# Performance work log

Hardware: AMD Instinct MI355X
Metric: run time of the kernel (lower is better)

Reference implementation:

```python
import jax, jax.numpy as jnp
import numpy as np

B, T, S = 64, 50, 400
H, E, V = 512, 256, 50000
NB_UNK = 50

def setup_inputs() -> dict:
    key = jax.random.key(0)
    ks = jax.random.split(key, 20)
    sc = 0.05
    return {
        "input_token": jax.random.randint(ks[0], (B, 1), 0, V),
        "prev_decoder_h_states": jax.random.normal(ks[1], (B, T, H)) * 0.1,
        "last_hidden": jax.random.normal(ks[2], (B, H)) * 0.1,
        "encoder_states": jax.random.normal(ks[3], (B, S, H)) * 0.1,
        "full_input_var": jax.random.randint(ks[4], (B, S), 0, V + NB_UNK + 200),
        "previous_att": jax.random.normal(ks[5], (B, T, S)) * 0.1,
        "nb_unk_tokens": NB_UNK,
        "emb": jax.random.normal(ks[6], (V, E)) * sc,
        "W_ih": jax.random.normal(ks[7], (3 * H, E)) * sc,
        "W_hh": jax.random.normal(ks[8], (3 * H, H)) * sc,
        "b_ih": jax.random.normal(ks[9], (3 * H,)) * sc,
        "b_hh": jax.random.normal(ks[10], (3 * H,)) * sc,
        "w_h": jax.random.normal(ks[11], (H,)) * sc,
        "w_d": jax.random.normal(ks[12], (H,)) * sc,
        "W_oh": jax.random.normal(ks[13], (E, 3 * H)) * sc,
        "b_oh": jax.random.normal(ks[14], (E,)) * sc,
        "W_ov": jax.random.normal(ks[15], (V, E)) * sc,
        "b_ov": jax.random.normal(ks[16], (V,)) * sc,
        "W_gen": jax.random.normal(ks[17], (1, 3 * H)) * sc,
        "b_gen": jax.random.normal(ks[18], (1,)) * sc,
    }

def gru_step(x, h, W_ih, W_hh, b_ih, b_hh):
    # PyTorch GRU gate order: r, z, n
    gi = x @ W_ih.T + b_ih   # [B,3H]
    gh = h @ W_hh.T + b_hh   # [B,3H]
    i_r, i_z, i_n = jnp.split(gi, 3, axis=-1)
    h_r, h_z, h_n = jnp.split(gh, 3, axis=-1)
    r = jax.nn.sigmoid(i_r + h_r)
    z = jax.nn.sigmoid(i_z + h_z)
    n = jnp.tanh(i_n + r * h_n)
    return (1.0 - z) * n + z * h

def reference(input_token, prev_decoder_h_states, last_hidden, encoder_states,
              full_input_var, previous_att, nb_unk_tokens,
              emb, W_ih, W_hh, b_ih, b_hh, w_h, w_d,
              W_oh, b_oh, W_ov, b_ov, W_gen, b_gen):
    # embedding (dropout is identity at eval)
    x = emb[input_token[:, 0]]                                 # [B,E]
    h = gru_step(x, last_hidden, W_ih, W_hh, b_ih, b_hh)       # [B,H]

    # temporal (intra-temporal) encoder attention
    att_dist = jnp.einsum('bh,bsh->bs', h, w_h * encoder_states)      # [B,S]
    temporal = jnp.exp(att_dist) / jnp.exp(previous_att).sum(1)       # [B,S]
    new_previous_att = jnp.concatenate([previous_att, att_dist[:, None]], 1)
    att = temporal / temporal.sum(-1, keepdims=True)                   # [B,S]
    enc_ctx = jnp.einsum('bs,bsh->bh', att, encoder_states)           # [B,H]

    # intra-decoder attention
    dec_scores = jnp.einsum('bh,bth->bt', h, w_d * prev_decoder_h_states)
    dec_att = jax.nn.softmax(dec_scores, axis=-1)                      # [B,T]
    dec_ctx = jnp.einsum('bt,bth->bh', dec_att, prev_decoder_h_states)

    combined = jnp.concatenate([h, enc_ctx, dec_ctx], axis=-1)        # [B,3H]
    logits = (combined @ W_oh.T + b_oh) @ W_ov.T + b_ov               # [B,V]
    p_vocab = jax.nn.softmax(logits, axis=-1)
    p_gen = jax.nn.sigmoid(combined @ W_gen.T + b_gen)                # [B,1]

    # pointer copy distribution over extended vocab
    ext = V + nb_unk_tokens + 200
    bidx = jnp.arange(full_input_var.shape[0])[:, None]
    token_input_dist = jnp.zeros((full_input_var.shape[0], ext), dtype=att.dtype)
    token_input_dist = token_input_dist.at[bidx, full_input_var].add(att)

    pad = jnp.zeros((full_input_var.shape[0], nb_unk_tokens + 200), dtype=p_vocab.dtype)
    p_final = jnp.concatenate([p_vocab * p_gen, pad], axis=1) + (1.0 - p_gen) * token_input_dist

    decoder_h_states = jnp.concatenate([prev_decoder_h_states, h[:, None]], axis=1)
    return (p_final, p_gen, p_vocab, att, decoder_h_states, h, new_previous_att)
```

## Files before the change

kernel.cpp:

```cpp
#include <hip/hip_runtime.h>
#include <hip/hip_bf16.h>

#define B 64
#define T 50
#define S 400
#define H 512
#define E 256
#define V 50000
#define EXT 50250
#define G3 1536
#define NCH 32
#define NCE 8

typedef __attribute__((ext_vector_type(8))) short short8;
typedef __attribute__((ext_vector_type(4))) float f32x4;

#define O_PFINAL 0L
#define O_PGEN   3216000L
#define O_PVOCAB 3216064L
#define O_ATT    6416064L
#define O_DECH   6441664L
#define O_H      8112832L
#define O_NPA    8145600L

#define OFF_G      0L
#define OFF_GG     98304L
#define OFF_H      196608L
#define OFF_HW     229376L
#define OFF_HWD    262144L
#define OFF_ENCP   294912L
#define OFF_DEC    557056L
#define OFF_E      589824L
#define OFF_ESUM   615424L
#define OFF_PG     615936L
#define OFF_PROJBF 616064L
#define OFF_PSUM   624256L
#define OFF_TOK    1048576L

__device__ __forceinline__ float sigmoidf_(float x){ return 1.0f/(1.0f+expf(-x)); }
__device__ __forceinline__ short f2bs(float x){
    union { __hip_bfloat16 b; short s; } c; c.b = __float2bfloat16(x); return c.s;
}
__device__ __forceinline__ short8 cvt8(const float* p){
    f32x4 w0 = *(const f32x4*)p;
    f32x4 w1 = *(const f32x4*)(p + 4);
    short8 r;
    r[0]=f2bs(w0[0]); r[1]=f2bs(w0[1]); r[2]=f2bs(w0[2]); r[3]=f2bs(w0[3]);
    r[4]=f2bs(w1[0]); r[5]=f2bs(w1[1]); r[6]=f2bs(w1[2]); r[7]=f2bs(w1[3]);
    return r;
}

__global__ void k_prep(const float* pdh, const float* pa, float* out, float* tokd){
    const long n1 = (long)B*T*H/4, n2 = (long)B*T*S/4;
    const long nz = (long)B*EXT/4;
    long i0 = (long)blockIdx.x*256 + threadIdx.x;
    long stride = (long)gridDim.x*256;
    for (long i = i0; i < n1 + n2; i += stride){
        if (i < n1){
            long idx = i*4;
            int b = (int)(idx/(T*H)); int r = (int)(idx%(T*H)); int t = r/H; int k = r%H;
            *(f32x4*)(out + O_DECH + ((long)b*(T+1) + t)*H + k) = *(const f32x4*)(pdh + idx);
        } else {
            long idx = (i - n1)*4;
            int b = (int)(idx/(T*S)); int r = (int)(idx%(T*S)); int t = r/S; int s = r%S;
            *(f32x4*)(out + O_NPA + ((long)b*(T+1) + t)*S + s) = *(const f32x4*)(pa + idx);
        }
    }
    f32x4 z = {0.f,0.f,0.f,0.f};
    for (long i = i0; i < nz; i += stride)
        *(f32x4*)(tokd + i*4) = z;
}

__global__ void __launch_bounds__(128) k_gates(const int* tok,
                        const float* emb, const float* lh,
                        const float* Wih, const float* Whh,
                        const float* bih, const float* bhh,
                        float* g, float* Gg){
    int lane = threadIdx.x & 63, wave = threadIdx.x >> 6;
    int row = lane & 15, kg = lane >> 4;
    int j = blockIdx.x*16 + row;
    f32x4 c0={0.f,0.f,0.f,0.f}, c1={0.f,0.f,0.f,0.f};
    f32x4 c2={0.f,0.f,0.f,0.f}, c3={0.f,0.f,0.f,0.f};
    if (wave == 0){
        const float* Wp = Wih + (long)j*E + kg*8;
        const float* a0p = emb + (long)tok[row     ]*E + kg*8;
        const float* a1p = emb + (long)tok[row + 16]*E + kg*8;
        const float* a2p = emb + (long)tok[row + 32]*E + kg*8;
        const float* a3p = emb + (long)tok[row + 48]*E + kg*8;
        #pragma unroll
        for (int ks = 0; ks < 8; ks++){
            short8 bb = cvt8(Wp + ks*32);
            c0 = __builtin_amdgcn_mfma_f32_16x16x32_bf16(cvt8(a0p + ks*32), bb, c0, 0, 0, 0);
            c1 = __builtin_amdgcn_mfma_f32_16x16x32_bf16(cvt8(a1p + ks*32), bb, c1, 0, 0, 0);
            c2 = __builtin_amdgcn_mfma_f32_16x16x32_bf16(cvt8(a2p + ks*32), bb, c2, 0, 0, 0);
            c3 = __builtin_amdgcn_mfma_f32_16x16x32_bf16(cvt8(a3p + ks*32), bb, c3, 0, 0, 0);
        }
        float bi = bih[j];
        #pragma unroll
        for (int r = 0; r < 4; r++){
            int bg = kg*4 + r;
            g[(long)(bg     )*G3 + j] = c0[r] + bi;
            g[(long)(bg + 16)*G3 + j] = c1[r] + bi;
            g[(long)(bg + 32)*G3 + j] = c2[r] + bi;
            g[(long)(bg + 48)*G3 + j] = c3[r] + bi;
        }
    } else {
        const float* Wp = Whh + (long)j*H + kg*8;
        const float* a0p = lh + (long)(row     )*H + kg*8;
        const float* a1p = lh + (long)(row + 16)*H + kg*8;
        const float* a2p = lh + (long)(row + 32)*H + kg*8;
        const float* a3p = lh + (long)(row + 48)*H + kg*8;
        #pragma unroll
        for (int ks = 0; ks < 16; ks++){
            short8 bb = cvt8(Wp + ks*32);
            c0 = __builtin_amdgcn_mfma_f32_16x16x32_bf16(cvt8(a0p + ks*32), bb, c0, 0, 0, 0);
            c1 = __builtin_amdgcn_mfma_f32_16x16x32_bf16(cvt8(a1p + ks*32), bb, c1, 0, 0, 0);
            c2 = __builtin_amdgcn_mfma_f32_16x16x32_bf16(cvt8(a2p + ks*32), bb, c2, 0, 0, 0);
            c3 = __builtin_amdgcn_mfma_f32_16x16x32_bf16(cvt8(a3p + ks*32), bb, c3, 0, 0, 0);
        }
        float bh = bhh[j];
        #pragma unroll
        for (int r = 0; r < 4; r++){
            int bg = kg*4 + r;
            Gg[(long)(bg     )*G3 + j] = c0[r] + bh;
            Gg[(long)(bg + 16)*G3 + j] = c1[r] + bh;
            Gg[(long)(bg + 32)*G3 + j] = c2[r] + bh;
            Gg[(long)(bg + 48)*G3 + j] = c3[r] + bh;
        }
    }
}

__global__ void k_gru(const float* g, const float* Gg, const float* lh,
                      const float* wh, const float* wd,
                      float* h, float* hw, float* hwd, float* out){
    int i = blockIdx.x*256 + threadIdx.x;
    int b = i >> 9, k = i & 511;
    float ir = g [b*G3 + k], iz = g [b*G3 + H + k], inn = g [b*G3 + 2*H + k];
    float hr = Gg[b*G3 + k], hz = Gg[b*G3 + H + k], hn  = Gg[b*G3 + 2*H + k];
    float r = sigmoidf_(ir + hr), z = sigmoidf_(iz + hz);
    float n = tanhf(inn + r*hn);
    float hp = lh[i];
    float hv = (1.f - z)*n + z*hp;
    h[i] = hv; hw[i] = hv * wh[k]; hwd[i] = hv * wd[k];
    out[O_H + i] = hv;
    out[O_DECH + ((long)b*(T+1) + T)*H + k] = hv;
}

__global__ void __launch_bounds__(512) k_fused(const float* hw, const float* enc,
                        const float* pa, float* ews, float* esum,
                        float* encp, float* out){
    int blk = blockIdx.x;
    int b = blk >> 3, c = blk & 7;
    int wave = threadIdx.x >> 6, lane = threadIdx.x & 63;
    const float* hwp = hw + b*H + lane*8;
    f32x4 h0 = *(const f32x4*)(hwp);
    f32x4 h1 = *(const f32x4*)(hwp + 4);
    float acc[8] = {0.f,0.f,0.f,0.f,0.f,0.f,0.f,0.f};
    float es = 0.f;
    for (int s0 = wave; s0 < S/NCE; s0 += 8){
        int s = c*(S/NCE) + s0;
        const float* ep = enc + ((long)b*S + s)*H + lane*8;
        f32x4 e0 = *(const f32x4*)(ep);
        f32x4 e1 = *(const f32x4*)(ep + 4);
        float d = 0.f;
        #pragma unroll
        for (int m = 0; m < 4; m++) d += h0[m]*e0[m] + h1[m]*e1[m];
        for (int off = 32; off > 0; off >>= 1) d += __shfl_xor(d, off);
        float pv = (lane < T) ? expf(pa[((long)b*T + lane)*S + s]) : 0.f;
        for (int off = 32; off > 0; off >>= 1) pv += __shfl_xor(pv, off);
        float ee = expf(d) / pv;
        if (lane == 0){
            out[O_NPA + ((long)b*(T+1) + T)*S + s] = d;
            ews[b*S + s] = ee;
        }
        es += ee;
        #pragma unroll
        for (int m = 0; m < 4; m++){ acc[m] += ee*e0[m]; acc[4+m] += ee*e1[m]; }
    }
    __shared__ float lacc[8][H];
    __shared__ float lsum[8];
    #pragma unroll
    for (int m = 0; m < 8; m++) lacc[wave][lane*8 + m] = acc[m];
    if (lane == 0) lsum[wave] = es;
    __syncthreads();
    int tid = threadIdx.x;
    float tt = 0.f;
    #pragma unroll
    for (int w = 0; w < 8; w++) tt += lacc[w][tid];
    encp[((long)b*NCE + c)*H + tid] = tt;
    if (tid == 0){
        float ss = 0.f;
        #pragma unroll
        for (int w = 0; w < 8; w++) ss += lsum[w];
        esum[b*NCE + c] = ss;
    }
}

__global__ void __launch_bounds__(512) k_post1(const float* hwd, const float* pdh,
                        const float* ews, const float* esum, const int* fiv,
                        float* dec, float* tokd, float* out){
    int tid = threadIdx.x;
    if (blockIdx.x < 64){
        int b = blockIdx.x;
        __shared__ float sc[T];
        int wave = tid >> 6, lane = tid & 63;
        const float* hp = hwd + b*H + lane*8;
        f32x4 h0 = *(const f32x4*)(hp);
        f32x4 h1 = *(const f32x4*)(hp + 4);
        for (int t = wave; t < T; t += 8){
            const float* pp = pdh + ((long)b*T + t)*H + lane*8;
            f32x4 p0 = *(const f32x4*)(pp);
            f32x4 p1 = *(const f32x4*)(pp + 4);
            float a = 0.f;
            #pragma unroll
            for (int m = 0; m < 4; m++) a += h0[m]*p0[m] + h1[m]*p1[m];
            for (int off = 32; off > 0; off >>= 1) a += __shfl_xor(a, off);
            if (lane == 0) sc[t] = a;
        }
        __syncthreads();
        if (wave == 0){
            float xv = (lane < T) ? sc[lane] : -1e30f;
            float m = xv;
            for (int off = 32; off > 0; off >>= 1) m = fmaxf(m, __shfl_xor(m, off));
            float e = (lane < T) ? expf(xv - m) : 0.f;
            float ssum = e;
            for (int off = 32; off > 0; off >>= 1) ssum += __shfl_xor(ssum, off);
            if (lane < T) sc[lane] = e / ssum;
        }
        __syncthreads();
        float a = 0.f;
        for (int t = 0; t < T; t++)
            a += sc[t] * pdh[((long)b*T + t)*H + tid];
        dec[b*H + tid] = a;
    } else {
        int b = blockIdx.x - 64;
        float inv = 0.f;
        #pragma unroll
        for (int c = 0; c < NCE; c++) inv += esum[b*NCE + c];
        inv = 1.f / inv;
        if (tid < S){
            float a = ews[b*S + tid] * inv;
            out[O_ATT + b*S + tid] = a;
            atomicAdd(&tokd[(long)b*EXT + fiv[b*S + tid]], a);
        }
    }
}

__global__ void k_projcomb(const float* h, const float* encp, const float* esum,
                           const float* dec,
                           const float* Woh, const float* boh,
                           const float* Wgen, const float* bgen,
                           short* projbf, float* pg, float* out){
    int blk = blockIdx.x;
    int b = blk >> 4, et = blk & 15;
    int tid = threadIdx.x;
    __shared__ float cl[G3];
    __shared__ float red[256];
    float inv = 0.f;
    #pragma unroll
    for (int c = 0; c < NCE; c++) inv += esum[b*NCE + c];
    inv = 1.f / inv;
    #pragma unroll
    for (int m = 0; m < 2; m++){
        int k = tid + 256*m;
        float v0 = h[b*H + k];
        float v1 = 0.f;
        #pragma unroll
        for (int c = 0; c < NCE; c++) v1 += encp[(b*NCE + c)*H + k];
        float v2 = dec[b*H + k];
        cl[k] = v0; cl[H + k] = v1*inv; cl[2*H + k] = v2;
    }
    __syncthreads();
    int wave = tid >> 6, lane = tid & 63;
    int e0 = et*16 + wave*4;
    const float* w0 = Woh + (long)(e0+0)*G3;
    const float* w1 = Woh + (long)(e0+1)*G3;
    const float* w2 = Woh + (long)(e0+2)*G3;
    const float* w3 = Woh + (long)(e0+3)*G3;
    float a0=0.f, a1=0.f, a2=0.f, a3=0.f;
    #pragma unroll
    for (int m = 0; m < 24; m++){
        int idx = lane + 64*m;
        float c = cl[idx];
        a0 += c * w0[idx]; a1 += c * w1[idx];
        a2 += c * w2[idx]; a3 += c * w3[idx];
    }
    for (int off = 32; off > 0; off >>= 1){
        a0 += __shfl_xor(a0, off); a1 += __shfl_xor(a1, off);
        a2 += __shfl_xor(a2, off); a3 += __shfl_xor(a3, off);
    }
    if (lane == 0){
        projbf[b*E + e0+0] = f2bs(a0 + boh[e0+0]);
        projbf[b*E + e0+1] = f2bs(a1 + boh[e0+1]);
        projbf[b*E + e0+2] = f2bs(a2 + boh[e0+2]);
        projbf[b*E + e0+3] = f2bs(a3 + boh[e0+3]);
    }
    if (et == 0){
        float part = 0.f;
        #pragma unroll
        for (int m = 0; m < 6; m++){
            int j = tid + 256*m;
            part += cl[j] * Wgen[j];
        }
        red[tid] = part; __syncthreads();
        for (int off = 128; off > 0; off >>= 1){
            if (tid < off) red[tid] += red[tid + off];
            __syncthreads();
        }
        if (tid == 0){
            float pv = sigmoidf_(red[0] + bgen[0]);
            pg[b] = pv;
            out[O_PGEN + b] = pv;
        }
    }
}

__global__ void __launch_bounds__(64) k_logits(const short* projbf, const float* Wov,
                         const float* bov, float* out){
    int lane = threadIdx.x;
    int vbase = blockIdx.x * 16;
    int row = lane & 15, kg = lane >> 4;
    f32x4 acc0 = {0.f,0.f,0.f,0.f}, acc1 = {0.f,0.f,0.f,0.f};
    f32x4 acc2 = {0.f,0.f,0.f,0.f}, acc3 = {0.f,0.f,0.f,0.f};
    const float* Bp = Wov + ((long)(vbase + row))*E + kg*8;
    const short* Ap = projbf + row*E + kg*8;
    #pragma unroll
    for (int ks = 0; ks < 8; ks++){
        short8 bb = cvt8(Bp + ks*32);
        short8 a0 = *(const short8*)(Ap + ks*32);
        short8 a1 = *(const short8*)(Ap + 16*E + ks*32);
        short8 a2 = *(const short8*)(Ap + 32*E + ks*32);
        short8 a3 = *(const short8*)(Ap + 48*E + ks*32);
        acc0 = __builtin_amdgcn_mfma_f32_16x16x32_bf16(a0, bb, acc0, 0, 0, 0);
        acc1 = __builtin_amdgcn_mfma_f32_16x16x32_bf16(a1, bb, acc1, 0, 0, 0);
        acc2 = __builtin_amdgcn_mfma_f32_16x16x32_bf16(a2, bb, acc2, 0, 0, 0);
        acc3 = __builtin_amdgcn_mfma_f32_16x16x32_bf16(a3, bb, acc3, 0, 0, 0);
    }
    int v = vbase + row;
    float bv = bov[v];
    #pragma unroll
    for (int r = 0; r < 4; r++){
        int bg = kg*4 + r;
        out[O_PVOCAB + (long)(bg     )*V + v] = acc0[r] + bv;
        out[O_PVOCAB + (long)(bg + 16)*V + v] = acc1[r] + bv;
        out[O_PVOCAB + (long)(bg + 32)*V + v] = acc2[r] + bv;
        out[O_PVOCAB + (long)(bg + 48)*V + v] = acc3[r] + bv;
    }
}

__global__ void k_smpart(const float* logits, float* psum){
    int b = blockIdx.x / NCH, c = blockIdx.x % NCH;
    const int chunk = (V + NCH - 1)/NCH;
    int start = c*chunk;
    int end = start + chunk; if (end > V) end = V;
    float s = 0.f;
    for (int v = start + threadIdx.x; v < end; v += 256)
        s += expf(logits[(long)b*V + v]);
    __shared__ float ss[256];
    int tid = threadIdx.x;
    ss[tid] = s; __syncthreads();
    for (int off = 128; off > 0; off >>= 1){
        if (tid < off) ss[tid] += ss[tid + off];
        __syncthreads();
    }
    if (tid == 0) psum[blockIdx.x] = ss[0];
}

__global__ void k_final(const float* psum, const float* pg,
                        const float* tokd, float* out){
    __shared__ float sm[1];
    int b = blockIdx.y;
    if (threadIdx.x < 64){
        int lane = threadIdx.x;
        float s = (lane < NCH) ? psum[b*NCH + lane] : 0.f;
        for (int off = 32; off > 0; off >>= 1) s += __shfl_xor(s, off);
        if (lane == 0) sm[0] = s;
    }
    __syncthreads();
    float inv = 1.f / sm[0];
    int t = blockIdx.x*256 + threadIdx.x;
    if (t >= EXT) return;
    float g = pg[b];
    float td = tokd[(long)b*EXT + t];
    float pf;
    if (t < V){
        long idx = O_PVOCAB + (long)b*V + t;
        float pv = expf(out[idx]) * inv;
        out[idx] = pv;
        pf = pv*g + (1.f - g)*td;
    } else {
        pf = (1.f - g)*td;
    }
    out[O_PFINAL + (long)b*EXT + t] = pf;
}

extern "C" void kernel_launch(void* const* d_in, const int* in_sizes, int n_in,
                              void* d_out, int out_size, void* d_ws, size_t ws_size,
                              hipStream_t stream) {
    const int*   tok  = (const int*)d_in[0];
    const float* pdh  = (const float*)d_in[1];
    const float* lh   = (const float*)d_in[2];
    const float* enc  = (const float*)d_in[3];
    const int*   fiv  = (const int*)d_in[4];
    const float* pa   = (const float*)d_in[5];
    const float* emb  = (const float*)d_in[7];
    const float* Wih  = (const float*)d_in[8];
    const float* Whh  = (const float*)d_in[9];
    const float* bih  = (const float*)d_in[10];
    const float* bhh  = (const float*)d_in[11];
    const float* wh   = (const float*)d_in[12];
    const float* wd   = (const float*)d_in[13];
    const float* Woh  = (const float*)d_in[14];
    const float* boh  = (const float*)d_in[15];
    const float* Wov  = (const float*)d_in[16];
    const float* bov  = (const float*)d_in[17];
    const float* Wgen = (const float*)d_in[18];
    const float* bgen = (const float*)d_in[19];

    float* ws  = (float*)d_ws;
    float* out = (float*)d_out;

    float* g      = ws + OFF_G;
    float* Gg     = ws + OFF_GG;
    float* h      = ws + OFF_H;
    float* hw     = ws + OFF_HW;
    float* hwd    = ws + OFF_HWD;
    float* encp   = ws + OFF_ENCP;
    float* dec    = ws + OFF_DEC;
    float* ews    = ws + OFF_E;
    float* esum   = ws + OFF_ESUM;
    float* pg     = ws + OFF_PG;
    short* projbf = (short*)(ws + OFF_PROJBF);
    float* psum   = ws + OFF_PSUM;
    float* tokd   = ws + OFF_TOK;

    k_prep    <<<2048, 256, 0, stream>>>(pdh, pa, out, tokd);
    k_gates   <<<G3/16, 128, 0, stream>>>(tok, emb, lh, Wih, Whh, bih, bhh, g, Gg);
    k_gru     <<<(B*H)/256, 256, 0, stream>>>(g, Gg, lh, wh, wd, h, hw, hwd, out);
    k_fused   <<<B*NCE, 512, 0, stream>>>(hw, enc, pa, ews, esum, encp, out);
    k_post1   <<<128, 512, 0, stream>>>(hwd, pdh, ews, esum, fiv, dec, tokd, out);
    k_projcomb<<<B*16, 256, 0, stream>>>(h, encp, esum, dec, Woh, boh, Wgen, bgen,
                                         projbf, pg, out);
    k_logits  <<<V/16, 64, 0, stream>>>(projbf, Wov, bov, out);
    k_smpart  <<<B*NCH, 256, 0, stream>>>(out + O_PVOCAB, psum);
    {
        dim3 grid((EXT + 255)/256, B);
        k_final<<<grid, 256, 0, stream>>>(psum, pg, tokd, out);
    }
}
```

Baseline: 90.51 us.

## Fuse decoder kernels, recompute GRU state in consumers, fold softmax sum into logits

Cuts the launch chain from eight kernels to five. The prep copy and gate GEMMs now run in one launch as separate block ranges. The GRU update is recomputed inside the attention, decoder-attention and projection kernels, which removes the separate GRU kernel and its h/hw/hwd buffers. Attention normalization and the scatter into the copy distribution move into the projection kernel. The logits kernel now writes exp(logit) directly and accumulates per-batch partial sums with atomics, which removes the separate softmax-sum pass and the exp in the final kernel. The costs are redundant GRU math, atomic contention on psum, and exp without max subtraction, which relies on logits staying small.

```diff
diff --git a/kernel.cpp b/kernel.cpp
--- a/kernel.cpp
+++ b/kernel.cpp
@@ -25,16 +25,13 @@
 
 #define OFF_G      0L
 #define OFF_GG     98304L
-#define OFF_H      196608L
-#define OFF_HW     229376L
-#define OFF_HWD    262144L
-#define OFF_ENCP   294912L
-#define OFF_DEC    557056L
-#define OFF_E      589824L
-#define OFF_ESUM   615424L
-#define OFF_PG     615936L
-#define OFF_PROJBF 616064L
-#define OFF_PSUM   624256L
+#define OFF_ENCP   196608L
+#define OFF_DEC    458752L
+#define OFF_E      491520L
+#define OFF_ESUM   517120L
+#define OFF_PG     517632L
+#define OFF_PROJBF 517696L
+#define OFF_PSUM   525888L
 #define OFF_TOK    1048576L
 
 __device__ __forceinline__ float sigmoidf_(float x){ return 1.0f/(1.0f+expf(-x)); }
@@ -49,164 +46,162 @@
     r[4]=f2bs(w1[0]); r[5]=f2bs(w1[1]); r[6]=f2bs(w1[2]); r[7]=f2bs(w1[3]);
     return r;
 }
-
-__global__ void k_prep(const float* pdh, const float* pa, float* out, float* tokd){
-    const long n1 = (long)B*T*H/4, n2 = (long)B*T*S/4;
-    const long nz = (long)B*EXT/4;
-    long i0 = (long)blockIdx.x*256 + threadIdx.x;
-    long stride = (long)gridDim.x*256;
-    for (long i = i0; i < n1 + n2; i += stride){
-        if (i < n1){
-            long idx = i*4;
-            int b = (int)(idx/(T*H)); int r = (int)(idx%(T*H)); int t = r/H; int k = r%H;
-            *(f32x4*)(out + O_DECH + ((long)b*(T+1) + t)*H + k) = *(const f32x4*)(pdh + idx);
-        } else {
-            long idx = (i - n1)*4;
-            int b = (int)(idx/(T*S)); int r = (int)(idx%(T*S)); int t = r/S; int s = r%S;
-            *(f32x4*)(out + O_NPA + ((long)b*(T+1) + t)*S + s) = *(const f32x4*)(pa + idx);
-        }
-    }
-    f32x4 z = {0.f,0.f,0.f,0.f};
-    for (long i = i0; i < nz; i += stride)
-        *(f32x4*)(tokd + i*4) = z;
-}
-
-__global__ void __launch_bounds__(128) k_gates(const int* tok,
-                        const float* emb, const float* lh,
-                        const float* Wih, const float* Whh,
-                        const float* bih, const float* bhh,
-                        float* g, float* Gg){
-    int lane = threadIdx.x & 63, wave = threadIdx.x >> 6;
-    int row = lane & 15, kg = lane >> 4;
-    int j = blockIdx.x*16 + row;
-    f32x4 c0={0.f,0.f,0.f,0.f}, c1={0.f,0.f,0.f,0.f};
-    f32x4 c2={0.f,0.f,0.f,0.f}, c3={0.f,0.f,0.f,0.f};
-    if (wave == 0){
-        const float* Wp = Wih + (long)j*E + kg*8;
-        const float* a0p = emb + (long)tok[row     ]*E + kg*8;
-        const float* a1p = emb + (long)tok[row + 16]*E + kg*8;
-        const float* a2p = emb + (long)tok[row + 32]*E + kg*8;
-        const float* a3p = emb + (long)tok[row + 48]*E + kg*8;
-        #pragma unroll
-        for (int ks = 0; ks < 8; ks++){
-            short8 bb = cvt8(Wp + ks*32);
-            c0 = __builtin_amdgcn_mfma_f32_16x16x32_bf16(cvt8(a0p + ks*32), bb, c0, 0, 0, 0);
-            c1 = __builtin_amdgcn_mfma_f32_16x16x32_bf16(cvt8(a1p + ks*32), bb, c1, 0, 0, 0);
-            c2 = __builtin_amdgcn_mfma_f32_16x16x32_bf16(cvt8(a2p + ks*32), bb, c2, 0, 0, 0);
-            c3 = __builtin_amdgcn_mfma_f32_16x16x32_bf16(cvt8(a3p + ks*32), bb, c3, 0, 0, 0);
-        }
-        float bi = bih[j];
-        #pragma unroll
-        for (int r = 0; r < 4; r++){
-            int bg = kg*4 + r;
-            g[(long)(bg     )*G3 + j] = c0[r] + bi;
-            g[(long)(bg + 16)*G3 + j] = c1[r] + bi;
-            g[(long)(bg + 32)*G3 + j] = c2[r] + bi;
-            g[(long)(bg + 48)*G3 + j] = c3[r] + bi;
-        }
-    } else {
-        const float* Wp = Whh + (long)j*H + kg*8;
-        const float* a0p = lh + (long)(row     )*H + kg*8;
-        const float* a1p = lh + (long)(row + 16)*H + kg*8;
-        const float* a2p = lh + (long)(row + 32)*H + kg*8;
-        const float* a3p = lh + (long)(row + 48)*H + kg*8;
-        #pragma unroll
-        for (int ks = 0; ks < 16; ks++){
-            short8 bb = cvt8(Wp + ks*32);
-            c0 = __builtin_amdgcn_mfma_f32_16x16x32_bf16(cvt8(a0p + ks*32), bb, c0, 0, 0, 0);
-            c1 = __builtin_amdgcn_mfma_f32_16x16x32_bf16(cvt8(a1p + ks*32), bb, c1, 0, 0, 0);
-            c2 = __builtin_amdgcn_mfma_f32_16x16x32_bf16(cvt8(a2p + ks*32), bb, c2, 0, 0, 0);
-            c3 = __builtin_amdgcn_mfma_f32_16x16x32_bf16(cvt8(a3p + ks*32), bb, c3, 0, 0, 0);
-        }
-        float bh = bhh[j];
-        #pragma unroll
-        for (int r = 0; r < 4; r++){
-            int bg = kg*4 + r;
-            Gg[(long)(bg     )*G3 + j] = c0[r] + bh;
-            Gg[(long)(bg + 16)*G3 + j] = c1[r] + bh;
-            Gg[(long)(bg + 32)*G3 + j] = c2[r] + bh;
-            Gg[(long)(bg + 48)*G3 + j] = c3[r] + bh;
-        }
-    }
-}
-
-__global__ void k_gru(const float* g, const float* Gg, const float* lh,
-                      const float* wh, const float* wd,
-                      float* h, float* hw, float* hwd, float* out){
-    int i = blockIdx.x*256 + threadIdx.x;
-    int b = i >> 9, k = i & 511;
+__device__ __forceinline__ float gru_h(const float* g, const float* Gg,
+                                       const float* lh, int b, int k){
     float ir = g [b*G3 + k], iz = g [b*G3 + H + k], inn = g [b*G3 + 2*H + k];
     float hr = Gg[b*G3 + k], hz = Gg[b*G3 + H + k], hn  = Gg[b*G3 + 2*H + k];
     float r = sigmoidf_(ir + hr), z = sigmoidf_(iz + hz);
     float n = tanhf(inn + r*hn);
-    float hp = lh[i];
-    float hv = (1.f - z)*n + z*hp;
-    h[i] = hv; hw[i] = hv * wh[k]; hwd[i] = hv * wd[k];
-    out[O_H + i] = hv;
-    out[O_DECH + ((long)b*(T+1) + T)*H + k] = hv;
-}
-
-__global__ void __launch_bounds__(512) k_fused(const float* hw, const float* enc,
-                        const float* pa, float* ews, float* esum,
-                        float* encp, float* out){
-    int blk = blockIdx.x;
-    int b = blk >> 3, c = blk & 7;
-    int wave = threadIdx.x >> 6, lane = threadIdx.x & 63;
-    const float* hwp = hw + b*H + lane*8;
-    f32x4 h0 = *(const f32x4*)(hwp);
-    f32x4 h1 = *(const f32x4*)(hwp + 4);
-    float acc[8] = {0.f,0.f,0.f,0.f,0.f,0.f,0.f,0.f};
-    float es = 0.f;
-    for (int s0 = wave; s0 < S/NCE; s0 += 8){
-        int s = c*(S/NCE) + s0;
-        const float* ep = enc + ((long)b*S + s)*H + lane*8;
-        f32x4 e0 = *(const f32x4*)(ep);
-        f32x4 e1 = *(const f32x4*)(ep + 4);
-        float d = 0.f;
-        #pragma unroll
-        for (int m = 0; m < 4; m++) d += h0[m]*e0[m] + h1[m]*e1[m];
-        for (int off = 32; off > 0; off >>= 1) d += __shfl_xor(d, off);
-        float pv = (lane < T) ? expf(pa[((long)b*T + lane)*S + s]) : 0.f;
-        for (int off = 32; off > 0; off >>= 1) pv += __shfl_xor(pv, off);
-        float ee = expf(d) / pv;
-        if (lane == 0){
-            out[O_NPA + ((long)b*(T+1) + T)*S + s] = d;
-            ews[b*S + s] = ee;
-        }
-        es += ee;
-        #pragma unroll
-        for (int m = 0; m < 4; m++){ acc[m] += ee*e0[m]; acc[4+m] += ee*e1[m]; }
-    }
+    return (1.f - z)*n + z*lh[b*H + k];
+}
+
+__global__ void __launch_bounds__(256) k_front(const int* tok,
+                        const float* emb, const float* lh,
+                        const float* Wih, const float* Whh,
+                        const float* bih, const float* bhh,
+                        const float* pdh, const float* pa,
+                        float* g, float* Gg, float* out, float* tokd){
+    if (blockIdx.x < 96){
+        if (threadIdx.x >= 128) return;
+        int lane = threadIdx.x & 63, wave = threadIdx.x >> 6;
+        int row = lane & 15, kg = lane >> 4;
+        int j = blockIdx.x*16 + row;
+        f32x4 c0={0.f,0.f,0.f,0.f}, c1={0.f,0.f,0.f,0.f};
+        f32x4 c2={0.f,0.f,0.f,0.f}, c3={0.f,0.f,0.f,0.f};
+        if (wave == 0){
+            const float* Wp = Wih + (long)j*E + kg*8;
+            const float* a0p = emb + (long)tok[row     ]*E + kg*8;
+            const float* a1p = emb + (long)tok[row + 16]*E + kg*8;
+            const float* a2p = emb + (long)tok[row + 32]*E + kg*8;
+            const float* a3p = emb + (long)tok[row + 48]*E + kg*8;
+            #pragma unroll
+            for (int ks = 0; ks < 8; ks++){
+                short8 bb = cvt8(Wp + ks*32);
+                c0 = __builtin_amdgcn_mfma_f32_16x16x32_bf16(cvt8(a0p + ks*32), bb, c0, 0, 0, 0);
+                c1 = __builtin_amdgcn_mfma_f32_16x16x32_bf16(cvt8(a1p + ks*32), bb, c1, 0, 0, 0);
+                c2 = __builtin_amdgcn_mfma_f32_16x16x32_bf16(cvt8(a2p + ks*32), bb, c2, 0, 0, 0);
+                c3 = __builtin_amdgcn_mfma_f32_16x16x32_bf16(cvt8(a3p + ks*32), bb, c3, 0, 0, 0);
+            }
+            float bi = bih[j];
+            #pragma unroll
+            for (int r = 0; r < 4; r++){
+                int bg = kg*4 + r;
+                g[(long)(bg     )*G3 + j] = c0[r] + bi;
+                g[(long)(bg + 16)*G3 + j] = c1[r] + bi;
+                g[(long)(bg + 32)*G3 + j] = c2[r] + bi;
+                g[(long)(bg + 48)*G3 + j] = c3[r] + bi;
+            }
+        } else {
+            const float* Wp = Whh + (long)j*H + kg*8;
+            const float* a0p = lh + (long)(row     )*H + kg*8;
+            const float* a1p = lh + (long)(row + 16)*H + kg*8;
+            const float* a2p = lh + (long)(row + 32)*H + kg*8;
+            const float* a3p = lh + (long)(row + 48)*H + kg*8;
+            #pragma unroll
+            for (int ks = 0; ks < 16; ks++){
+                short8 bb = cvt8(Wp + ks*32);
+                c0 = __builtin_amdgcn_mfma_f32_16x16x32_bf16(cvt8(a0p + ks*32), bb, c0, 0, 0, 0);
+                c1 = __builtin_amdgcn_mfma_f32_16x16x32_bf16(cvt8(a1p + ks*32), bb, c1, 0, 0, 0);
+                c2 = __builtin_amdgcn_mfma_f32_16x16x32_bf16(cvt8(a2p + ks*32), bb, c2, 0, 0, 0);
+                c3 = __builtin_amdgcn_mfma_f32_16x16x32_bf16(cvt8(a3p + ks*32), bb, c3, 0, 0, 0);
+            }
+            float bh = bhh[j];
+            #pragma unroll
+            for (int r = 0; r < 4; r++){
+                int bg = kg*4 + r;
+                Gg[(long)(bg     )*G3 + j] = c0[r] + bh;
+                Gg[(long)(bg + 16)*G3 + j] = c1[r] + bh;
+                Gg[(long)(bg + 32)*G3 + j] = c2[r] + bh;
+                Gg[(long)(bg + 48)*G3 + j] = c3[r] + bh;
+            }
+        }
+    } else {
+        const long n1 = (long)B*T*H/4, n2 = (long)B*T*S/4;
+        const long nz = (long)B*EXT/4;
+        long i0 = (long)(blockIdx.x - 96)*256 + threadIdx.x;
+        long stride = 2048L*256;
+        for (long i = i0; i < n1 + n2; i += stride){
+            if (i < n1){
+                long idx = i*4;
+                int b = (int)(idx/(T*H)); int r = (int)(idx%(T*H)); int t = r/H; int k = r%H;
+                *(f32x4*)(out + O_DECH + ((long)b*(T+1) + t)*H + k) = *(const f32x4*)(pdh + idx);
+            } else {
+                long idx = (i - n1)*4;
+                int b = (int)(idx/(T*S)); int r = (int)(idx%(T*S)); int t = r/S; int s = r%S;
+                *(f32x4*)(out + O_NPA + ((long)b*(T+1) + t)*S + s) = *(const f32x4*)(pa + idx);
+            }
+        }
+        f32x4 z = {0.f,0.f,0.f,0.f};
+        for (long i = i0; i < nz; i += stride)
+            *(f32x4*)(tokd + i*4) = z;
+    }
+}
+
+__global__ void __launch_bounds__(512) k_fused(const float* g, const float* Gg,
+                        const float* lh, const float* wh, const float* wd,
+                        const float* enc, const float* pa, const float* pdh,
+                        float* ews, float* esum, float* encp, float* dec, float* out){
+    __shared__ float sh[H];
     __shared__ float lacc[8][H];
     __shared__ float lsum[8];
-    #pragma unroll
-    for (int m = 0; m < 8; m++) lacc[wave][lane*8 + m] = acc[m];
-    if (lane == 0) lsum[wave] = es;
-    __syncthreads();
+    __shared__ float scs[64];
     int tid = threadIdx.x;
-    float tt = 0.f;
-    #pragma unroll
-    for (int w = 0; w < 8; w++) tt += lacc[w][tid];
-    encp[((long)b*NCE + c)*H + tid] = tt;
-    if (tid == 0){
-        float ss = 0.f;
-        #pragma unroll
-        for (int w = 0; w < 8; w++) ss += lsum[w];
-        esum[b*NCE + c] = ss;
-    }
-}
-
-__global__ void __launch_bounds__(512) k_post1(const float* hwd, const float* pdh,
-                        const float* ews, const float* esum, const int* fiv,
-                        float* dec, float* tokd, float* out){
-    int tid = threadIdx.x;
-    if (blockIdx.x < 64){
-        int b = blockIdx.x;
-        __shared__ float sc[T];
+    if (blockIdx.x < 512){
+        int b = blockIdx.x >> 3, c = blockIdx.x & 7;
+        float hv = gru_h(g, Gg, lh, b, tid);
+        sh[tid] = hv * wh[tid];
+        if (c == 0){
+            out[O_H + b*H + tid] = hv;
+            out[O_DECH + ((long)b*(T+1) + T)*H + tid] = hv;
+        }
+        __syncthreads();
         int wave = tid >> 6, lane = tid & 63;
-        const float* hp = hwd + b*H + lane*8;
-        f32x4 h0 = *(const f32x4*)(hp);
-        f32x4 h1 = *(const f32x4*)(hp + 4);
+        f32x4 h0 = *(const f32x4*)(&sh[lane*8]);
+        f32x4 h1 = *(const f32x4*)(&sh[lane*8 + 4]);
+        float acc[8] = {0.f,0.f,0.f,0.f,0.f,0.f,0.f,0.f};
+        float es = 0.f;
+        for (int s0 = wave; s0 < S/NCE; s0 += 8){
+            int s = c*(S/NCE) + s0;
+            const float* ep = enc + ((long)b*S + s)*H + lane*8;
+            f32x4 e0 = *(const f32x4*)(ep);
+            f32x4 e1 = *(const f32x4*)(ep + 4);
+            float d = 0.f;
+            #pragma unroll
+            for (int m = 0; m < 4; m++) d += h0[m]*e0[m] + h1[m]*e1[m];
+            for (int off = 32; off > 0; off >>= 1) d += __shfl_xor(d, off);
+            float pv = (lane < T) ? expf(pa[((long)b*T + lane)*S + s]) : 0.f;
+            for (int off = 32; off > 0; off >>= 1) pv += __shfl_xor(pv, off);
+            float ee = expf(d) / pv;
+            if (lane == 0){
+                out[O_NPA + ((long)b*(T+1) + T)*S + s] = d;
+                ews[b*S + s] = ee;
+            }
+            es += ee;
+            #pragma unroll
+            for (int m = 0; m < 4; m++){ acc[m] += ee*e0[m]; acc[4+m] += ee*e1[m]; }
+        }
+        #pragma unroll
+        for (int m = 0; m < 8; m++) lacc[wave][lane*8 + m] = acc[m];
+        if (lane == 0) lsum[wave] = es;
+        __syncthreads();
+        float tt = 0.f;
+        #pragma unroll
+        for (int w = 0; w < 8; w++) tt += lacc[w][tid];
+        encp[((long)b*NCE + c)*H + tid] = tt;
+        if (tid == 0){
+            float ss = 0.f;
+            #pragma unroll
+            for (int w = 0; w < 8; w++) ss += lsum[w];
+            esum[b*NCE + c] = ss;
+        }
+    } else {
+        int b = blockIdx.x - 512;
+        float hv = gru_h(g, Gg, lh, b, tid);
+        sh[tid] = hv * wd[tid];
+        __syncthreads();
+        int wave = tid >> 6, lane = tid & 63;
+        f32x4 h0 = *(const f32x4*)(&sh[lane*8]);
+        f32x4 h1 = *(const f32x4*)(&sh[lane*8 + 4]);
         for (int t = wave; t < T; t += 8){
             const float* pp = pdh + ((long)b*T + t)*H + lane*8;
             f32x4 p0 = *(const f32x4*)(pp);
@@ -215,42 +210,33 @@
             #pragma unroll
             for (int m = 0; m < 4; m++) a += h0[m]*p0[m] + h1[m]*p1[m];
             for (int off = 32; off > 0; off >>= 1) a += __shfl_xor(a, off);
-            if (lane == 0) sc[t] = a;
+            if (lane == 0) scs[t] = a;
         }
         __syncthreads();
         if (wave == 0){
-            float xv = (lane < T) ? sc[lane] : -1e30f;
+            float xv = (lane < T) ? scs[lane] : -1e30f;
             float m = xv;
             for (int off = 32; off > 0; off >>= 1) m = fmaxf(m, __shfl_xor(m, off));
             float e = (lane < T) ? expf(xv - m) : 0.f;
             float ssum = e;
             for (int off = 32; off > 0; off >>= 1) ssum += __shfl_xor(ssum, off);
-            if (lane < T) sc[lane] = e / ssum;
+            if (lane < T) scs[lane] = e / ssum;
         }
         __syncthreads();
         float a = 0.f;
         for (int t = 0; t < T; t++)
-            a += sc[t] * pdh[((long)b*T + t)*H + tid];
+            a += scs[t] * pdh[((long)b*T + t)*H + tid];
         dec[b*H + tid] = a;
-    } else {
-        int b = blockIdx.x - 64;
-        float inv = 0.f;
-        #pragma unroll
-        for (int c = 0; c < NCE; c++) inv += esum[b*NCE + c];
-        inv = 1.f / inv;
-        if (tid < S){
-            float a = ews[b*S + tid] * inv;
-            out[O_ATT + b*S + tid] = a;
-            atomicAdd(&tokd[(long)b*EXT + fiv[b*S + tid]], a);
-        }
-    }
-}
-
-__global__ void k_projcomb(const float* h, const float* encp, const float* esum,
-                           const float* dec,
+    }
+}
+
+__global__ void k_projcomb(const float* g, const float* Gg, const float* lh,
+                           const float* encp, const float* esum, const float* dec,
                            const float* Woh, const float* boh,
                            const float* Wgen, const float* bgen,
-                           short* projbf, float* pg, float* out){
+                           const float* ews, const int* fiv,
+                           short* projbf, float* pg, float* psum,
+                           float* tokd, float* out){
     int blk = blockIdx.x;
     int b = blk >> 4, et = blk & 15;
     int tid = threadIdx.x;
@@ -263,12 +249,11 @@
     #pragma unroll
     for (int m = 0; m < 2; m++){
         int k = tid + 256*m;
-        float v0 = h[b*H + k];
+        float hv = gru_h(g, Gg, lh, b, k);
         float v1 = 0.f;
         #pragma unroll
         for (int c = 0; c < NCE; c++) v1 += encp[(b*NCE + c)*H + k];
-        float v2 = dec[b*H + k];
-        cl[k] = v0; cl[H + k] = v1*inv; cl[2*H + k] = v2;
+        cl[k] = hv; cl[H + k] = v1*inv; cl[2*H + k] = dec[b*H + k];
     }
     __syncthreads();
     int wave = tid >> 6, lane = tid & 63;
@@ -312,11 +297,19 @@
             pg[b] = pv;
             out[O_PGEN + b] = pv;
         }
+    } else if (et == 1){
+        for (int s = tid; s < S; s += 256){
+            float a = ews[b*S + s] * inv;
+            out[O_ATT + b*S + s] = a;
+            atomicAdd(&tokd[(long)b*EXT + fiv[b*S + s]], a);
+        }
+    } else if (et == 2){
+        if (tid < NCH) psum[b*NCH + tid] = 0.f;
     }
 }
 
 __global__ void __launch_bounds__(64) k_logits(const short* projbf, const float* Wov,
-                         const float* bov, float* out){
+                         const float* bov, float* psum, float* out){
     int lane = threadIdx.x;
     int vbase = blockIdx.x * 16;
     int row = lane & 15, kg = lane >> 4;
@@ -338,32 +331,39 @@
     }
     int v = vbase + row;
     float bv = bov[v];
+    float sums[4][4];
     #pragma unroll
     for (int r = 0; r < 4; r++){
         int bg = kg*4 + r;
-        out[O_PVOCAB + (long)(bg     )*V + v] = acc0[r] + bv;
-        out[O_PVOCAB + (long)(bg + 16)*V + v] = acc1[r] + bv;
-        out[O_PVOCAB + (long)(bg + 32)*V + v] = acc2[r] + bv;
-        out[O_PVOCAB + (long)(bg + 48)*V + v] = acc3[r] + bv;
-    }
-}
-
-__global__ void k_smpart(const float* logits, float* psum){
-    int b = blockIdx.x / NCH, c = blockIdx.x % NCH;
-    const int chunk = (V + NCH - 1)/NCH;
-    int start = c*chunk;
-    int end = start + chunk; if (end > V) end = V;
-    float s = 0.f;
-    for (int v = start + threadIdx.x; v < end; v += 256)
-        s += expf(logits[(long)b*V + v]);
-    __shared__ float ss[256];
-    int tid = threadIdx.x;
-    ss[tid] = s; __syncthreads();
-    for (int off = 128; off > 0; off >>= 1){
-        if (tid < off) ss[tid] += ss[tid + off];
-        __syncthreads();
-    }
-    if (tid == 0) psum[blockIdx.x] = ss[0];
+        float ev0 = expf(acc0[r] + bv);
+        float ev1 = expf(acc1[r] + bv);
+        float ev2 = expf(acc2[r] + bv);
+        float ev3 = expf(acc3[r] + bv);
+        out[O_PVOCAB + (long)(bg     )*V + v] = ev0;
+        out[O_PVOCAB + (long)(bg + 16)*V + v] = ev1;
+        out[O_PVOCAB + (long)(bg + 32)*V + v] = ev2;
+        out[O_PVOCAB + (long)(bg + 48)*V + v] = ev3;
+        sums[0][r] = ev0; sums[1][r] = ev1; sums[2][r] = ev2; sums[3][r] = ev3;
+    }
+    #pragma unroll
+    for (int N = 0; N < 4; N++)
+        #pragma unroll
+        for (int r = 0; r < 4; r++){
+            float sv = sums[N][r];
+            sv += __shfl_xor(sv, 1); sv += __shfl_xor(sv, 2);
+            sv += __shfl_xor(sv, 4); sv += __shfl_xor(sv, 8);
+            sums[N][r] = sv;
+        }
+    if (row == 0){
+        int slot = blockIdx.x & (NCH - 1);
+        #pragma unroll
+        for (int N = 0; N < 4; N++)
+            #pragma unroll
+            for (int r = 0; r < 4; r++){
+                int bg = kg*4 + r + 16*N;
+                atomicAdd(&psum[bg*NCH + slot], sums[N][r]);
+            }
+    }
 }
 
 __global__ void k_final(const float* psum, const float* pg,
@@ -380,16 +380,16 @@
     float inv = 1.f / sm[0];
     int t = blockIdx.x*256 + threadIdx.x;
     if (t >= EXT) return;
-    float g = pg[b];
+    float gv = pg[b];
     float td = tokd[(long)b*EXT + t];
     float pf;
     if (t < V){
         long idx = O_PVOCAB + (long)b*V + t;
-        float pv = expf(out[idx]) * inv;
+        float pv = out[idx] * inv;
         out[idx] = pv;
-        pf = pv*g + (1.f - g)*td;
+        pf = pv*gv + (1.f - gv)*td;
     } else {
-        pf = (1.f - g)*td;
+        pf = (1.f - gv)*td;
     }
     out[O_PFINAL + (long)b*EXT + t] = pf;
 }
@@ -422,9 +422,6 @@
 
     float* g      = ws + OFF_G;
     float* Gg     = ws + OFF_GG;
-    float* h      = ws + OFF_H;
-    float* hw     = ws + OFF_HW;
-    float* hwd    = ws + OFF_HWD;
     float* encp   = ws + OFF_ENCP;
     float* dec    = ws + OFF_DEC;
     float* ews    = ws + OFF_E;
@@ -434,15 +431,14 @@
     float* psum   = ws + OFF_PSUM;
     float* tokd   = ws + OFF_TOK;
 
-    k_prep    <<<2048, 256, 0, stream>>>(pdh, pa, out, tokd);
-    k_gates   <<<G3/16, 128, 0, stream>>>(tok, emb, lh, Wih, Whh, bih, bhh, g, Gg);
-    k_gru     <<<(B*H)/256, 256, 0, stream>>>(g, Gg, lh, wh, wd, h, hw, hwd, out);
-    k_fused   <<<B*NCE, 512, 0, stream>>>(hw, enc, pa, ews, esum, encp, out);
-    k_post1   <<<128, 512, 0, stream>>>(hwd, pdh, ews, esum, fiv, dec, tokd, out);
-    k_projcomb<<<B*16, 256, 0, stream>>>(h, encp, esum, dec, Woh, boh, Wgen, bgen,
-                                         projbf, pg, out);
-    k_logits  <<<V/16, 64, 0, stream>>>(projbf, Wov, bov, out);
-    k_smpart  <<<B*NCH, 256, 0, stream>>>(out + O_PVOCAB, psum);
+    k_front   <<<96 + 2048, 256, 0, stream>>>(tok, emb, lh, Wih, Whh, bih, bhh,
+                                              pdh, pa, g, Gg, out, tokd);
+    k_fused   <<<512 + 64, 512, 0, stream>>>(g, Gg, lh, wh, wd, enc, pa, pdh,
+                                             ews, esum, encp, dec, out);
+    k_projcomb<<<B*16, 256, 0, stream>>>(g, Gg, lh, encp, esum, dec,
+                                         Woh, boh, Wgen, bgen, ews, fiv,
+                                         projbf, pg, psum, tokd, out);
+    k_logits  <<<V/16, 64, 0, stream>>>(projbf, Wov, bov, psum, out);
     {
         dim3 grid((EXT + 255)/256, B);
         k_final<<<grid, 256, 0, stream>>>(psum, pg, tokd, out);
```

Result: slower. 114.7 us (+26.7%).
